# Performance work log

Measured on AMD Instinct MI355X. Metric: run time of the kernel, lower is better.

The kernel has to match this reference:

```python
import jax, jax.numpy as jnp
import numpy as np

ACT = jax.nn.leaky_relu  # Decima uses leaky_relu activations


def _mlp(x, params):
    # Linear + act chain (activation applied after every layer, incl. last, as in the torch code)
    for W, b in params:
        x = ACT(x @ W + b)
    return x


def setup_inputs() -> dict:
    key = jax.random.key(0)
    N, E, D = 500_000, 4_000_000, 8  # nodes, edges per depth, max_depth
    ks = jax.random.split(key, 32)
    inp = {}
    inp["inputs"] = jax.random.normal(ks[0], (N, 5), dtype=jnp.float32)
    inp["adj_src"] = jax.random.randint(ks[1], (D, E), 0, N, dtype=jnp.int32)
    inp["adj_dst"] = jax.random.randint(ks[2], (D, E), 0, N, dtype=jnp.int32)
    inp["masks"] = (jax.random.uniform(ks[3], (D, N, 1)) > 0.5).astype(jnp.float32)
    # MLP stacks: prep 5->16->32->8, proc/agg 8->16->32->8 (xavier-ish init, zero bias)
    dims = {"prep": [(5, 16), (16, 32), (32, 8)],
            "proc": [(8, 16), (16, 32), (32, 8)],
            "agg": [(8, 16), (16, 32), (32, 8)]}
    i = 4
    for name, ds in dims.items():
        for j, (a, b) in enumerate(ds):
            scale = np.sqrt(6.0 / (a + b)).astype(np.float32)
            inp[f"{name}_W{j}"] = jax.random.uniform(ks[i], (a, b), jnp.float32, -scale, scale)
            inp[f"{name}_b{j}"] = jnp.zeros((b,), jnp.float32)
            i += 1
    return inp


def reference(inputs, adj_src, adj_dst, masks,
              prep_W0, prep_b0, prep_W1, prep_b1, prep_W2, prep_b2,
              proc_W0, proc_b0, proc_W1, proc_b1, proc_W2, proc_b2,
              agg_W0, agg_b0, agg_W1, agg_b1, agg_W2, agg_b2):
    prep = [(prep_W0, prep_b0), (prep_W1, prep_b1), (prep_W2, prep_b2)]
    proc = [(proc_W0, proc_b0), (proc_W1, proc_b1), (proc_W2, proc_b2)]
    agg = [(agg_W0, agg_b0), (agg_W1, agg_b1), (agg_W2, agg_b2)]
    N = inputs.shape[0]
    max_depth = adj_src.shape[0]

    x = _mlp(inputs, prep)  # [N, 8]
    for d in range(max_depth):  # small fixed loop over depths
        y = _mlp(x, proc)  # [N, 8]
        # sparse adj matmul (unit-valued adjacency): out[i] = sum_{j: (i,j) in adj} y[j]
        y = jax.ops.segment_sum(y[adj_src[d]], adj_dst[d], num_segments=N)
        y = _mlp(y, agg)
        x = x + y * masks[d]  # mask + residual
    return x
```

## Files before the change

### kernel.cpp

```cpp
#include <hip/hip_runtime.h>
#include <hip/hip_fp16.h>


typedef unsigned long long u64;
typedef unsigned int u32;

#define BKT_BITS 10
#define BKT_SIZE 1024
#define MAXNB    512
#define NBLK     256

template <int CH> struct Cfg;
template <> struct Cfg<4> { static const int CAPC = 6;  static const int SUBC = 24; };
template <> struct Cfg<2> { static const int CAPC = 14; static const int SUBC = 32; };
template <> struct Cfg<1> { static const int CAPC = 30; static const int SUBC = 64; };

__device__ __forceinline__ float lrelu(float v) { return fmaxf(v, 0.01f * v); }

template <int IN>
__device__ __forceinline__ void mlp3(const float* __restrict__ xin, float* __restrict__ yout,
    const float* __restrict__ sW0, const float* __restrict__ sb0,
    const float* __restrict__ sW1, const float* __restrict__ sb1,
    const float* __restrict__ sW2, const float* __restrict__ sb2)
{
    float h1[16];
#pragma unroll
    for (int o = 0; o < 16; ++o) {
        float s = sb0[o];
#pragma unroll
        for (int a = 0; a < IN; ++a) s = fmaf(xin[a], sW0[a * 16 + o], s);
        h1[o] = lrelu(s);
    }
    float h2[32];
#pragma unroll
    for (int o = 0; o < 32; ++o) {
        float s = sb1[o];
#pragma unroll
        for (int a = 0; a < 16; ++a) s = fmaf(h1[a], sW1[a * 32 + o], s);
        h2[o] = lrelu(s);
    }
#pragma unroll
    for (int o = 0; o < 8; ++o) {
        float s = sb2[o];
#pragma unroll
        for (int a = 0; a < 32; ++a) s = fmaf(h2[a], sW2[a * 8 + o], s);
        yout[o] = lrelu(s);
    }
}

__device__ __forceinline__ void ldw(float* d, const float* s, int n) {
    for (int t = threadIdx.x; t < n; t += 256) d[t] = s[t];
}

__device__ __forceinline__ uint4 pack_h8(const float* y) {
    __half2 p0 = __floats2half2_rn(y[0], y[1]);
    __half2 p1 = __floats2half2_rn(y[2], y[3]);
    __half2 p2 = __floats2half2_rn(y[4], y[5]);
    __half2 p3 = __floats2half2_rn(y[6], y[7]);
    uint4 v;
    v.x = *(u32*)&p0; v.y = *(u32*)&p1; v.z = *(u32*)&p2; v.w = *(u32*)&p3;
    return v;
}

__global__ __launch_bounds__(256) void prep_proc_kernel(
    const float* __restrict__ in, float* __restrict__ x, uint4* __restrict__ y,
    const float* pW0, const float* pb0, const float* pW1, const float* pb1,
    const float* pW2, const float* pb2,
    const float* cW0, const float* cb0, const float* cW1, const float* cb1,
    const float* cW2, const float* cb2, int N)
{
    __shared__ float P0[80],  Pb0[16], P1[512], Pb1[32], P2[256], Pb2[8];
    __shared__ float C0[128], Cb0[16], C1[512], Cb1[32], C2[256], Cb2[8];
    ldw(P0, pW0, 80);  ldw(Pb0, pb0, 16); ldw(P1, pW1, 512); ldw(Pb1, pb1, 32);
    ldw(P2, pW2, 256); ldw(Pb2, pb2, 8);
    ldw(C0, cW0, 128); ldw(Cb0, cb0, 16); ldw(C1, cW1, 512); ldw(Cb1, cb1, 32);
    ldw(C2, cW2, 256); ldw(Cb2, cb2, 8);
    __syncthreads();
    int i = blockIdx.x * 256 + threadIdx.x;
    if (i >= N) return;
    float xin[5];
#pragma unroll
    for (int k = 0; k < 5; ++k) xin[k] = in[(size_t)i * 5 + k];
    float xv[8];
    mlp3<5>(xin, xv, P0, Pb0, P1, Pb1, P2, Pb2);
    float4* xp = (float4*)(x + 8 * (size_t)i);
    xp[0] = make_float4(xv[0], xv[1], xv[2], xv[3]);
    xp[1] = make_float4(xv[4], xv[5], xv[6], xv[7]);
    float yv[8];
    mlp3<8>(xv, yv, C0, Cb0, C1, Cb1, C2, Cb2);
    y[i] = pack_h8(yv);
}

template <bool DO_PROC, int CHUNKS>
__global__ __launch_bounds__(256) void aggproc_kernel(
    const uint4* __restrict__ acc, float* __restrict__ x, const float* __restrict__ mask,
    uint4* __restrict__ y,
    const float* aW0, const float* ab0, const float* aW1, const float* ab1,
    const float* aW2, const float* ab2,
    const float* cW0, const float* cb0, const float* cW1, const float* cb1,
    const float* cW2, const float* cb2, int N)
{
    __shared__ float A0[128], Ab0[16], A1[512], Ab1[32], A2[256], Ab2[8];
    __shared__ float C0[128], Cb0[16], C1[512], Cb1[32], C2[256], Cb2[8];
    ldw(A0, aW0, 128); ldw(Ab0, ab0, 16); ldw(A1, aW1, 512); ldw(Ab1, ab1, 32);
    ldw(A2, aW2, 256); ldw(Ab2, ab2, 8);
    if (DO_PROC) {
        ldw(C0, cW0, 128); ldw(Cb0, cb0, 16); ldw(C1, cW1, 512); ldw(Cb1, cb1, 32);
        ldw(C2, cW2, 256); ldw(Cb2, cb2, 8);
    }
    __syncthreads();
    int i = blockIdx.x * 256 + threadIdx.x;
    if (i >= N) return;
    float ain[8] = {0.f, 0.f, 0.f, 0.f, 0.f, 0.f, 0.f, 0.f};
#pragma unroll
    for (int c = 0; c < CHUNKS; ++c) {
        uint4 v = acc[(size_t)c * N + i];
        float2 f0 = __half22float2(*(__half2*)&v.x);
        float2 f1 = __half22float2(*(__half2*)&v.y);
        float2 f2 = __half22float2(*(__half2*)&v.z);
        float2 f3 = __half22float2(*(__half2*)&v.w);
        ain[0] += f0.x; ain[1] += f0.y; ain[2] += f1.x; ain[3] += f1.y;
        ain[4] += f2.x; ain[5] += f2.y; ain[6] += f3.x; ain[7] += f3.y;
    }
    float ya[8];
    mlp3<8>(ain, ya, A0, Ab0, A1, Ab1, A2, Ab2);
    float m = mask[i];
    float4* xp = (float4*)(x + 8 * (size_t)i);
    float4 x0 = xp[0], x1 = xp[1];
    float xn[8] = {x0.x + ya[0] * m, x0.y + ya[1] * m, x0.z + ya[2] * m, x0.w + ya[3] * m,
                   x1.x + ya[4] * m, x1.y + ya[5] * m, x1.z + ya[6] * m, x1.w + ya[7] * m};
    xp[0] = make_float4(xn[0], xn[1], xn[2], xn[3]);
    xp[1] = make_float4(xn[4], xn[5], xn[6], xn[7]);
    if (DO_PROC) {
        float yv[8];
        mlp3<8>(xn, yv, C0, Cb0, C1, Cb1, C2, Cb2);
        y[i] = pack_h8(yv);
    }
}

__global__ __launch_bounds__(256) void mask_pack_kernel(
    const float* __restrict__ masks, u64* __restrict__ bitmaps, int N, int D, int BITW)
{
    int i = blockIdx.x * 256 + threadIdx.x;
    int lane = threadIdx.x & 63;
    for (int d = 0; d < D; ++d) {
        bool b = (i < N) ? (masks[(size_t)d * N + i] != 0.f) : false;
        u64 m = __ballot(b);
        if (lane == 0 && i < N) bitmaps[(size_t)d * BITW + (i >> 6)] = m;
    }
}

template <int CHUNKS>
__global__ __launch_bounds__(256) void place_kernel(
    const int* __restrict__ src, const int* __restrict__ dst,
    const u64* __restrict__ bitmap,
    u32* __restrict__ ebuf,
    int* __restrict__ cnt_g,
    int E, int NB, int shift)
{
    constexpr int CAPC = Cfg<CHUNKS>::CAPC;
    constexpr int SUBC = Cfg<CHUNKS>::SUBC;
    __shared__ int lcnt[MAXNB * CHUNKS];
    __shared__ u32 stage[MAXNB * CHUNKS * CAPC];
    const int cells = NB * CHUNKS;
    for (int t = threadIdx.x; t < cells; t += 256) lcnt[t] = 0;
    __syncthreads();

    const int blk = blockIdx.x;
    const int E4 = E >> 2;
    const int CH4 = (E4 + NBLK - 1) / NBLK;
    const int base4 = blk * CH4;
    const int lim4 = min(base4 + CH4, E4);
    const int4* src4 = (const int4*)src;
    const int4* dst4 = (const int4*)dst;

#define PLACE(dv, sv) { int _d = (dv); \
    if ((bitmap[_d >> 6] >> (_d & 63)) & 1ull) { \
        int _cell = (_d >> BKT_BITS) * CHUNKS + ((u32)(sv) >> shift); \
        int _slot = atomicAdd(&lcnt[_cell], 1); \
        u32 _w = ((u32)(sv) << BKT_BITS) | (u32)(_d & (BKT_SIZE - 1)); \
        if (_slot < CAPC) stage[_cell * CAPC + _slot] = _w; \
        else if (_slot < SUBC) ebuf[((size_t)_cell * NBLK + blk) * SUBC + _slot] = _w; \
    } }

    for (int i4 = base4 + threadIdx.x; i4 < lim4; i4 += 256) {
        int4 dv = dst4[i4];
        int4 sv = src4[i4];
        PLACE(dv.x, sv.x) PLACE(dv.y, sv.y) PLACE(dv.z, sv.z) PLACE(dv.w, sv.w)
    }
    if (blk == NBLK - 1)
        for (int e = (E4 << 2) + threadIdx.x; e < E; e += 256) { PLACE(dst[e], src[e]) }
#undef PLACE

    __syncthreads();
    constexpr int SLOTW = (CAPC <= 8) ? 8 : (CAPC <= 16) ? 16 : 32;
    constexpr int CPW = 64 / SLOTW;
    int wave = threadIdx.x >> 6, lane = threadIdx.x & 63;
    int cslot = lane % SLOTW, coff = lane / SLOTW;
    for (int c0 = wave * CPW; c0 < cells; c0 += 4 * CPW) {
        int cell = c0 + coff;
        if (cell < cells) {
            int n = lcnt[cell];
            int ns = min(n, CAPC);
            size_t gb = ((size_t)cell * NBLK + blk) * SUBC;
            if (cslot < ns) ebuf[gb + cslot] = stage[cell * CAPC + cslot];
            if (cslot == 0) cnt_g[cell * NBLK + blk] = min(n, SUBC);
        }
    }
}

__device__ __forceinline__ void accum4(__half2* __restrict__ sacc, u32 w, uint4 v)
{
    int dl = (int)(w & (BKT_SIZE - 1));
    __half2* a = sacc + dl * 5;
    unsafeAtomicAdd(a + 0, *(__half2*)&v.x);
    unsafeAtomicAdd(a + 1, *(__half2*)&v.y);
    unsafeAtomicAdd(a + 2, *(__half2*)&v.z);
    unsafeAtomicAdd(a + 3, *(__half2*)&v.w);
}

template <int CHUNKS>
__global__ __launch_bounds__(256) void reduce_kernel(
    const uint4* __restrict__ y, const u32* __restrict__ ebuf, const int* __restrict__ cnt_g,
    uint4* __restrict__ acc, int N, int NB)
{
    constexpr int SUBC = Cfg<CHUNKS>::SUBC;
    int i = blockIdx.x, bucket, chunk;
    if (CHUNKS == 4)      { bucket = (i >> 3) * 2 + (i & 1); chunk = (i >> 1) & 3; }
    else if (CHUNKS == 2) { bucket = (i >> 3) * 4 + (i & 3); chunk = (i >> 2) & 1; }
    else                  { bucket = i; chunk = 0; }
    if (bucket >= NB) return;

    __shared__ __half2 sacc[BKT_SIZE * 5];
    for (int t = threadIdx.x; t < BKT_SIZE * 5; t += 256) ((u32*)sacc)[t] = 0u;
    __syncthreads();

    int cell = bucket * CHUNKS + chunk;
    int sb = cell * NBLK + threadIdx.x;
    int n = cnt_g[sb];
    const u32* r = ebuf + (size_t)sb * SUBC;

    int k = 0;
    for (; k + 3 < n; k += 4) {
        u32 w0 = r[k], w1 = r[k + 1], w2 = r[k + 2], w3 = r[k + 3];
        uint4 v0 = y[w0 >> BKT_BITS];
        uint4 v1 = y[w1 >> BKT_BITS];
        uint4 v2 = y[w2 >> BKT_BITS];
        uint4 v3 = y[w3 >> BKT_BITS];
        accum4(sacc, w0, v0);
        accum4(sacc, w1, v1);
        accum4(sacc, w2, v2);
        accum4(sacc, w3, v3);
    }
    for (; k < n; ++k) {
        u32 w = r[k];
        uint4 v = y[w >> BKT_BITS];
        accum4(sacc, w, v);
    }

    __syncthreads();
    int node0 = bucket << BKT_BITS;
    uint4* accc = acc + (size_t)chunk * N;
    for (int t = threadIdx.x; t < BKT_SIZE; t += 256) {
        int idx = node0 + t;
        if (idx < N) {
            __half2* a = sacc + t * 5;
            uint4 o;
            o.x = *(u32*)(a + 0); o.y = *(u32*)(a + 1);
            o.z = *(u32*)(a + 2); o.w = *(u32*)(a + 3);
            accc[idx] = o;
        }
    }
}

__global__ __launch_bounds__(256) void scatter_kernel(
    const uint4* __restrict__ y, const int* __restrict__ src, const int* __restrict__ dst,
    const float* __restrict__ mask, __half2* __restrict__ acc, int E)
{
    int e = blockIdx.x * blockDim.x + threadIdx.x;
    if (e >= E) return;
    int d = dst[e];
    if (mask[d] == 0.f) return;
    int s = src[e];
    uint4 v = y[s];
    __half2* o = acc + 4 * (size_t)d;
    unsafeAtomicAdd(o + 0, *(__half2*)&v.x);
    unsafeAtomicAdd(o + 1, *(__half2*)&v.y);
    unsafeAtomicAdd(o + 2, *(__half2*)&v.z);
    unsafeAtomicAdd(o + 3, *(__half2*)&v.w);
}

template <int CH>
static void run_depth(hipStream_t stream, bool last, int N, int E, int NB, int shift, int nbN,
                      const int* src_d, const int* dst_d, const u64* bitmap_d,
                      u32* ebuf, int* cnt_g, uint4* y, uint4* acc, float* x, const float* mask_d,
                      const float* aW0, const float* ab0, const float* aW1, const float* ab1,
                      const float* aW2, const float* ab2,
                      const float* cW0, const float* cb0, const float* cW1, const float* cb1,
                      const float* cW2, const float* cb2)
{
    place_kernel<CH><<<NBLK, 256, 0, stream>>>(src_d, dst_d, bitmap_d, ebuf, cnt_g, E, NB, shift);
    int rgrid = (CH == 4) ? ((NB + 1) / 2) * 8 : (CH == 2) ? ((NB + 3) / 4) * 8 : NB;
    reduce_kernel<CH><<<rgrid, 256, 0, stream>>>(y, ebuf, cnt_g, acc, N, NB);
    if (!last)
        aggproc_kernel<true, CH><<<nbN, 256, 0, stream>>>(acc, x, mask_d, y,
            aW0, ab0, aW1, ab1, aW2, ab2, cW0, cb0, cW1, cb1, cW2, cb2, N);
    else
        aggproc_kernel<false, CH><<<nbN, 256, 0, stream>>>(acc, x, mask_d, y,
            aW0, ab0, aW1, ab1, aW2, ab2, cW0, cb0, cW1, cb1, cW2, cb2, N);
}

extern "C" void kernel_launch(void* const* d_in, const int* in_sizes, int n_in,
                              void* d_out, int out_size, void* d_ws, size_t ws_size,
                              hipStream_t stream)
{
    const float* inputs  = (const float*)d_in[0];
    const int*   adj_src = (const int*)d_in[1];
    const int*   adj_dst = (const int*)d_in[2];
    const float* masks   = (const float*)d_in[3];

    const float* pW0 = (const float*)d_in[4];  const float* pb0 = (const float*)d_in[5];
    const float* pW1 = (const float*)d_in[6];  const float* pb1 = (const float*)d_in[7];
    const float* pW2 = (const float*)d_in[8];  const float* pb2 = (const float*)d_in[9];
    const float* cW0 = (const float*)d_in[10]; const float* cb0 = (const float*)d_in[11];
    const float* cW1 = (const float*)d_in[12]; const float* cb1 = (const float*)d_in[13];
    const float* cW2 = (const float*)d_in[14]; const float* cb2 = (const float*)d_in[15];
    const float* aW0 = (const float*)d_in[16]; const float* ab0 = (const float*)d_in[17];
    const float* aW1 = (const float*)d_in[18]; const float* ab1 = (const float*)d_in[19];
    const float* aW2 = (const float*)d_in[20]; const float* ab2 = (const float*)d_in[21];

    const int N = in_sizes[0] / 5;
    const int D = in_sizes[3] / N;
    const int E = in_sizes[1] / D;
    const int NB = (N + BKT_SIZE - 1) >> BKT_BITS;
    const int BITW = (N + 63) >> 6;

    float* x = (float*)d_out;

    auto layout_bytes = [&](int ch) -> size_t {
        int subc = (ch == 4) ? 24 : (ch == 2) ? 32 : 64;
        size_t s = 0;
        auto al = [&](size_t b) { s = (s + b + 255) & ~(size_t)255; };
        al((size_t)N * 16);
        al((size_t)ch * N * 16);
        al((size_t)D * BITW * 8);
        al((size_t)NB * ch * NBLK * subc * 4);
        al((size_t)NB * ch * NBLK * 4);
        return s;
    };
    int CHsel = 0;
    if (NB <= MAXNB) {
        if (layout_bytes(4) <= ws_size) CHsel = 4;
        else if (layout_bytes(2) <= ws_size) CHsel = 2;
        else if (layout_bytes(1) <= ws_size) CHsel = 1;
    }
    bool fast = CHsel > 0;
    int subc = (CHsel == 4) ? 24 : (CHsel == 2) ? 32 : 64;

    char* w = (char*)d_ws;
    size_t off = 0;
    auto take = [&](size_t bytes) { char* p = w + off; off = (off + bytes + 255) & ~(size_t)255; return p; };
    uint4* y   = (uint4*)take((size_t)N * 16);
    uint4* acc = (uint4*)take((size_t)(fast ? CHsel : 1) * N * 16);
    u64* bitmaps = (u64*)take((size_t)D * BITW * 8);
    u32* ebuf  = fast ? (u32*)take((size_t)NB * CHsel * NBLK * subc * 4) : nullptr;
    int* cnt_g = fast ? (int*)take((size_t)NB * CHsel * NBLK * 4) : nullptr;

    int shift = 0;
    if (fast) { while ((u32)(N - 1) >> shift >= (u32)CHsel) shift++; }

    const int BLK = 256;
    const int nbN = (N + BLK - 1) / BLK;
    const int nbE = (E + BLK - 1) / BLK;

    if (fast)
        mask_pack_kernel<<<nbN, BLK, 0, stream>>>(masks, bitmaps, N, D, BITW);

    prep_proc_kernel<<<nbN, BLK, 0, stream>>>(inputs, x, y,
                                              pW0, pb0, pW1, pb1, pW2, pb2,
                                              cW0, cb0, cW1, cb1, cW2, cb2, N);

    for (int d = 0; d < D; ++d) {
        const float* mask_d = masks + (size_t)d * N;
        const int* src_d = adj_src + (size_t)d * E;
        const int* dst_d = adj_dst + (size_t)d * E;
        bool last = (d == D - 1);

        if (fast) {
            const u64* bm = bitmaps + (size_t)d * BITW;
            if (CHsel == 4)
                run_depth<4>(stream, last, N, E, NB, shift, nbN, src_d, dst_d, bm, ebuf, cnt_g,
                             y, acc, x, mask_d, aW0, ab0, aW1, ab1, aW2, ab2,
                             cW0, cb0, cW1, cb1, cW2, cb2);
            else if (CHsel == 2)
                run_depth<2>(stream, last, N, E, NB, shift, nbN, src_d, dst_d, bm, ebuf, cnt_g,
                             y, acc, x, mask_d, aW0, ab0, aW1, ab1, aW2, ab2,
                             cW0, cb0, cW1, cb1, cW2, cb2);
            else
                run_depth<1>(stream, last, N, E, NB, shift, nbN, src_d, dst_d, bm, ebuf, cnt_g,
                             y, acc, x, mask_d, aW0, ab0, aW1, ab1, aW2, ab2,
                             cW0, cb0, cW1, cb1, cW2, cb2);
        } else {
            hipMemsetAsync(acc, 0, (size_t)N * 16, stream);
            scatter_kernel<<<nbE, BLK, 0, stream>>>(y, src_d, dst_d, mask_d, (__half2*)acc, E);
            if (!last)
                aggproc_kernel<true, 1><<<nbN, BLK, 0, stream>>>(acc, x, mask_d, y,
                    aW0, ab0, aW1, ab1, aW2, ab2, cW0, cb0, cW1, cb1, cW2, cb2, N);
            else
                aggproc_kernel<false, 1><<<nbN, BLK, 0, stream>>>(acc, x, mask_d, y,
                    aW0, ab0, aW1, ab1, aW2, ab2, cW0, cb0, cW1, cb1, cW2, cb2, N);
        }
    }
}
```

Before: 1.373 ms.

## Batch edge bucketing across all depths into one place kernel launch

```diff
diff --git a/kernel.cpp b/kernel.cpp
--- a/kernel.cpp
+++ b/kernel.cpp
@@ -152,14 +152,21 @@
 
 template <int CHUNKS>
 __global__ __launch_bounds__(256) void place_kernel(
-    const int* __restrict__ src, const int* __restrict__ dst,
-    const u64* __restrict__ bitmap,
-    u32* __restrict__ ebuf,
-    int* __restrict__ cnt_g,
-    int E, int NB, int shift)
+    const int* __restrict__ adj_src, const int* __restrict__ adj_dst,
+    const u64* __restrict__ bitmaps,
+    u32* __restrict__ ebuf_all,
+    int* __restrict__ cnt_all,
+    int E, int NB, int shift, int BITW)
 {
     constexpr int CAPC = Cfg<CHUNKS>::CAPC;
     constexpr int SUBC = Cfg<CHUNKS>::SUBC;
+    const int dep = blockIdx.y;
+    const int* src = adj_src + (size_t)dep * E;
+    const int* dst = adj_dst + (size_t)dep * E;
+    const u64* bitmap = bitmaps + (size_t)dep * BITW;
+    u32* ebuf = ebuf_all + (size_t)dep * ((size_t)NB * CHUNKS * NBLK * SUBC);
+    int* cnt_g = cnt_all + (size_t)dep * ((size_t)NB * CHUNKS * NBLK);
+
     __shared__ int lcnt[MAXNB * CHUNKS];
     __shared__ u32 stage[MAXNB * CHUNKS * CAPC];
     const int cells = NB * CHUNKS;
@@ -291,23 +298,41 @@
 }
 
 template <int CH>
-static void run_depth(hipStream_t stream, bool last, int N, int E, int NB, int shift, int nbN,
-                      const int* src_d, const int* dst_d, const u64* bitmap_d,
-                      u32* ebuf, int* cnt_g, uint4* y, uint4* acc, float* x, const float* mask_d,
-                      const float* aW0, const float* ab0, const float* aW1, const float* ab1,
-                      const float* aW2, const float* ab2,
-                      const float* cW0, const float* cb0, const float* cW1, const float* cb1,
-                      const float* cW2, const float* cb2)
-{
-    place_kernel<CH><<<NBLK, 256, 0, stream>>>(src_d, dst_d, bitmap_d, ebuf, cnt_g, E, NB, shift);
-    int rgrid = (CH == 4) ? ((NB + 1) / 2) * 8 : (CH == 2) ? ((NB + 3) / 4) * 8 : NB;
-    reduce_kernel<CH><<<rgrid, 256, 0, stream>>>(y, ebuf, cnt_g, acc, N, NB);
-    if (!last)
-        aggproc_kernel<true, CH><<<nbN, 256, 0, stream>>>(acc, x, mask_d, y,
-            aW0, ab0, aW1, ab1, aW2, ab2, cW0, cb0, cW1, cb1, cW2, cb2, N);
-    else
-        aggproc_kernel<false, CH><<<nbN, 256, 0, stream>>>(acc, x, mask_d, y,
-            aW0, ab0, aW1, ab1, aW2, ab2, cW0, cb0, cW1, cb1, cW2, cb2, N);
+static void run_fast(hipStream_t stream, bool batch, int N, int E, int D, int NB, int shift,
+                     int BITW, int nbN,
+                     const int* adj_src, const int* adj_dst, const float* masks,
+                     const u64* bitmaps, u32* ebuf, int* cnt_g,
+                     uint4* y, uint4* acc, float* x,
+                     const float* aW0, const float* ab0, const float* aW1, const float* ab1,
+                     const float* aW2, const float* ab2,
+                     const float* cW0, const float* cb0, const float* cW1, const float* cb1,
+                     const float* cW2, const float* cb2)
+{
+    constexpr int SUBC = Cfg<CH>::SUBC;
+    const size_t EB = (size_t)NB * CH * NBLK * SUBC;
+    const size_t CN = (size_t)NB * CH * NBLK;
+    const int rgrid = (CH == 4) ? ((NB + 1) / 2) * 8 : (CH == 2) ? ((NB + 3) / 4) * 8 : NB;
+
+    if (batch)
+        place_kernel<CH><<<dim3(NBLK, D), 256, 0, stream>>>(adj_src, adj_dst, bitmaps,
+                                                            ebuf, cnt_g, E, NB, shift, BITW);
+
+    for (int d = 0; d < D; ++d) {
+        const float* mask_d = masks + (size_t)d * N;
+        if (!batch)
+            place_kernel<CH><<<dim3(NBLK, 1), 256, 0, stream>>>(
+                adj_src + (size_t)d * E, adj_dst + (size_t)d * E, bitmaps + (size_t)d * BITW,
+                ebuf, cnt_g, E, NB, shift, BITW);
+        const u32* eb_d = ebuf + (batch ? (size_t)d * EB : 0);
+        const int* cg_d = cnt_g + (batch ? (size_t)d * CN : 0);
+        reduce_kernel<CH><<<rgrid, 256, 0, stream>>>(y, eb_d, cg_d, acc, N, NB);
+        if (d < D - 1)
+            aggproc_kernel<true, CH><<<nbN, 256, 0, stream>>>(acc, x, mask_d, y,
+                aW0, ab0, aW1, ab1, aW2, ab2, cW0, cb0, cW1, cb1, cW2, cb2, N);
+        else
+            aggproc_kernel<false, CH><<<nbN, 256, 0, stream>>>(acc, x, mask_d, y,
+                aW0, ab0, aW1, ab1, aW2, ab2, cW0, cb0, cW1, cb1, cW2, cb2, N);
+    }
 }
 
 extern "C" void kernel_launch(void* const* d_in, const int* in_sizes, int n_in,
@@ -337,25 +362,28 @@
 
     float* x = (float*)d_out;
 
-    auto layout_bytes = [&](int ch) -> size_t {
+    auto layout_bytes = [&](int ch, bool batch) -> size_t {
         int subc = (ch == 4) ? 24 : (ch == 2) ? 32 : 64;
+        int nd = batch ? D : 1;
         size_t s = 0;
         auto al = [&](size_t b) { s = (s + b + 255) & ~(size_t)255; };
         al((size_t)N * 16);
         al((size_t)ch * N * 16);
         al((size_t)D * BITW * 8);
-        al((size_t)NB * ch * NBLK * subc * 4);
-        al((size_t)NB * ch * NBLK * 4);
+        al((size_t)nd * NB * ch * NBLK * subc * 4);
+        al((size_t)nd * NB * ch * NBLK * 4);
         return s;
     };
-    int CHsel = 0;
+    int CHsel = 0; bool batch = false;
     if (NB <= MAXNB) {
-        if (layout_bytes(4) <= ws_size) CHsel = 4;
-        else if (layout_bytes(2) <= ws_size) CHsel = 2;
-        else if (layout_bytes(1) <= ws_size) CHsel = 1;
+        struct Opt { int ch; bool b; };
+        const Opt opts[6] = {{4,true},{2,true},{1,true},{4,false},{2,false},{1,false}};
+        for (int k = 0; k < 6; ++k)
+            if (layout_bytes(opts[k].ch, opts[k].b) <= ws_size) { CHsel = opts[k].ch; batch = opts[k].b; break; }
     }
     bool fast = CHsel > 0;
     int subc = (CHsel == 4) ? 24 : (CHsel == 2) ? 32 : 64;
+    int nd = batch ? D : 1;
 
     char* w = (char*)d_ws;
     size_t off = 0;
@@ -363,8 +391,8 @@
     uint4* y   = (uint4*)take((size_t)N * 16);
     uint4* acc = (uint4*)take((size_t)(fast ? CHsel : 1) * N * 16);
     u64* bitmaps = (u64*)take((size_t)D * BITW * 8);
-    u32* ebuf  = fast ? (u32*)take((size_t)NB * CHsel * NBLK * subc * 4) : nullptr;
-    int* cnt_g = fast ? (int*)take((size_t)NB * CHsel * NBLK * 4) : nullptr;
+    u32* ebuf  = fast ? (u32*)take((size_t)nd * NB * CHsel * NBLK * subc * 4) : nullptr;
+    int* cnt_g = fast ? (int*)take((size_t)nd * NB * CHsel * NBLK * 4) : nullptr;
 
     int shift = 0;
     if (fast) { while ((u32)(N - 1) >> shift >= (u32)CHsel) shift++; }
@@ -380,27 +408,25 @@
                                               pW0, pb0, pW1, pb1, pW2, pb2,
                                               cW0, cb0, cW1, cb1, cW2, cb2, N);
 
-    for (int d = 0; d < D; ++d) {
-        const float* mask_d = masks + (size_t)d * N;
-        const int* src_d = adj_src + (size_t)d * E;
-        const int* dst_d = adj_dst + (size_t)d * E;
-        bool last = (d == D - 1);
-
-        if (fast) {
-            const u64* bm = bitmaps + (size_t)d * BITW;
-            if (CHsel == 4)
-                run_depth<4>(stream, last, N, E, NB, shift, nbN, src_d, dst_d, bm, ebuf, cnt_g,
-                             y, acc, x, mask_d, aW0, ab0, aW1, ab1, aW2, ab2,
-                             cW0, cb0, cW1, cb1, cW2, cb2);
-            else if (CHsel == 2)
-                run_depth<2>(stream, last, N, E, NB, shift, nbN, src_d, dst_d, bm, ebuf, cnt_g,
-                             y, acc, x, mask_d, aW0, ab0, aW1, ab1, aW2, ab2,
-                             cW0, cb0, cW1, cb1, cW2, cb2);
-            else
-                run_depth<1>(stream, last, N, E, NB, shift, nbN, src_d, dst_d, bm, ebuf, cnt_g,
-                             y, acc, x, mask_d, aW0, ab0, aW1, ab1, aW2, ab2,
-                             cW0, cb0, cW1, cb1, cW2, cb2);
-        } else {
+    if (fast) {
+        if (CHsel == 4)
+            run_fast<4>(stream, batch, N, E, D, NB, shift, BITW, nbN, adj_src, adj_dst, masks,
+                        bitmaps, ebuf, cnt_g, y, acc, x,
+                        aW0, ab0, aW1, ab1, aW2, ab2, cW0, cb0, cW1, cb1, cW2, cb2);
+        else if (CHsel == 2)
+            run_fast<2>(stream, batch, N, E, D, NB, shift, BITW, nbN, adj_src, adj_dst, masks,
+                        bitmaps, ebuf, cnt_g, y, acc, x,
+                        aW0, ab0, aW1, ab1, aW2, ab2, cW0, cb0, cW1, cb1, cW2, cb2);
+        else
+            run_fast<1>(stream, batch, N, E, D, NB, shift, BITW, nbN, adj_src, adj_dst, masks,
+                        bitmaps, ebuf, cnt_g, y, acc, x,
+                        aW0, ab0, aW1, ab1, aW2, ab2, cW0, cb0, cW1, cb1, cW2, cb2);
+    } else {
+        for (int d = 0; d < D; ++d) {
+            const float* mask_d = masks + (size_t)d * N;
+            const int* src_d = adj_src + (size_t)d * E;
+            const int* dst_d = adj_dst + (size_t)d * E;
+            bool last = (d == D - 1);
             hipMemsetAsync(acc, 0, (size_t)N * 16, stream);
             scatter_kernel<<<nbE, BLK, 0, stream>>>(y, src_d, dst_d, mask_d, (__half2*)acc, E);
             if (!last)
```

New measurement: 1.345 ms. 1.02x faster.
